# Optimization experiments

Measured on AMD Instinct MI355X. Metric: run time of the kernel, lower is better.

## Reference

```python
import jax, jax.numpy as jnp
import numpy as np


def channel_linear(h, W, b):
    # h: (b, s, n_in, d_channels); W: (d, n_out, n_in); b: (d, n_out)
    out = jnp.einsum('bsic,coi->bsoc', h, W)
    return out + b.T[None, None]  # (b, s, n_out, d)


def setup_inputs() -> dict:
    d, s, bsz = 64, 64, 512
    lt, p = d * (d - 1) // 2, d * d
    key = jax.random.key(0)
    ks = jax.random.split(key, 12)
    inp = {
        'x': jax.random.normal(ks[0], (bsz, d), dtype=jnp.float32),
        'z': jax.random.normal(ks[1], (s, lt + p), dtype=jnp.float32),
    }
    widths = [d, 32, 32, 32, 1]
    for li, (ni, no) in enumerate(zip(widths[:-1], widths[1:])):
        inp[f'W{li}'] = jax.random.normal(ks[2 + 2 * li], (d, no, ni), dtype=jnp.float32) / np.sqrt(ni).astype(np.float32)
        inp[f'b{li}'] = jax.random.normal(ks[3 + 2 * li], (d, no), dtype=jnp.float32) * 0.01
    return inp


def reference(x, z, W0, b0, W1, b1, W2, b2, W3, b3):
    d = x.shape[1]
    s = z.shape[0]
    lt_width = d * (d - 1) // 2
    rows, cols = np.tril_indices(d, -1)  # matches torch.tril_indices(d, d, offset=-1)

    # get_z_adjacency_lt_p: strictly-lower-triangular matrix conjugated by z_p
    z_lt = jnp.zeros((s, d, d), dtype=z.dtype).at[:, rows, cols].set(z[:, :lt_width])
    z_p = z[:, -d * d:].reshape(s, d, d)
    # z_p^T @ z_lt @ z_p
    z_adj = jnp.einsum('sri,srt,stj->sij', z_p, z_lt, z_p)  # (s, d, d)

    # broadcast multiply: h[b,s,i,j] = A[s,i,j] * x[b,i]
    h = z_adj[None, :, :, :] * x[:, None, :, None]  # (b, s, d, d)

    h = jax.nn.relu(channel_linear(h, W0, b0))  # (b, s, 32, d)
    h = jax.nn.relu(channel_linear(h, W1, b1))
    h = jax.nn.relu(channel_linear(h, W2, b2))
    out = jnp.squeeze(channel_linear(h, W3, b3), axis=-2)  # (b, s, d)
    return (out, z_adj)
```

## Files before the change

### kernel.cpp

```cpp
#include <hip/hip_runtime.h>
#include <math.h>

#define D 64
#define S 64
#define BSZ 512
#define LTW 2016
#define ZROW 6112
#define OUT0_SIZE (BSZ * S * D)
#define ZADJ_OFF  OUT0_SIZE

typedef float    f32x4 __attribute__((ext_vector_type(4)));
typedef _Float16 f16x8 __attribute__((ext_vector_type(8)));
typedef _Float16 f16x2 __attribute__((ext_vector_type(2)));

union V8 { f16x8 v; f16x2 h2[4]; uint4 u; };

__device__ __forceinline__ f16x2 pkrtz(float a, float b) {
    return __builtin_bit_cast(f16x2, __builtin_amdgcn_cvt_pkrtz(a, b));
}

__global__ __launch_bounds__(256) void k_zadjprep(
    const float* __restrict__ z, float* __restrict__ zadj,
    const float* __restrict__ x,
    const float* __restrict__ W0, const float* __restrict__ W1,
    const float* __restrict__ W2,
    uint4* __restrict__ w0f, uint4* __restrict__ w1f,
    uint4* __restrict__ w2f, uint4* __restrict__ xf) {
    __shared__ float zp[4096];
    __shared__ float zlt[4160];
    __shared__ float T[1280];
    const int blk = blockIdx.x;
    const int tid = threadIdx.x;

    if (blk < 256) {
        const int s = blk >> 2, jt = blk & 3;
        const float* zs = z + (size_t)s * ZROW;
#pragma unroll
        for (int rep = 0; rep < 16; ++rep) {
            int idx = tid + rep * 256;
            zp[idx] = zs[LTW + idx];
        }
        for (int idx = tid; idx < 4160; idx += 256) zlt[idx] = 0.0f;
        __syncthreads();
        for (int k = tid; k < LTW; k += 256) {
            float kf = (float)k;
            int r = (int)((1.0f + sqrtf(1.0f + 8.0f * kf)) * 0.5f);
            while (r * (r - 1) / 2 > k) --r;
            while ((r + 1) * r / 2 <= k) ++r;
            int t = k - r * (r - 1) / 2;
            zlt[r * 65 + t] = zs[k];
        }
        __syncthreads();
        const int rr = tid & 63, wj = (tid >> 6) * 4;
        {
            f32x4 acc = {0.0f, 0.0f, 0.0f, 0.0f};
            for (int t = 0; t < 64; ++t) {
                float zl = zlt[rr * 65 + t];
                f32x4 zpv = *(const f32x4*)&zp[t * 64 + jt * 16 + wj];
#pragma unroll
                for (int q = 0; q < 4; ++q) acc[q] = fmaf(zl, zpv[q], acc[q]);
            }
            *(f32x4*)&T[rr * 20 + wj] = acc;
        }
        __syncthreads();
        {
            const int i = rr;
            f32x4 acc = {0.0f, 0.0f, 0.0f, 0.0f};
            for (int r = 0; r < 64; ++r) {
                float zv = zp[r * 64 + i];
                f32x4 tv = *(const f32x4*)&T[r * 20 + wj];
#pragma unroll
                for (int q = 0; q < 4; ++q) acc[q] = fmaf(zv, tv[q], acc[q]);
            }
            *(f32x4*)&zadj[(size_t)s * 4096 + i * 64 + jt * 16 + wj] = acc;
        }
    } else {
        const int c = blk - 256;
        const int sl = tid >> 6, ln = tid & 63;
        const int q = ln >> 4, l15 = ln & 15;
        {
            int Mt = sl >> 1, ks = sl & 1;
            const float* src = W0 + c * 2048 + (Mt * 16 + l15) * 64 + ks * 32 + q * 8;
            V8 hv;
#pragma unroll
            for (int j = 0; j < 8; ++j) hv.v[j] = (_Float16)src[j];
            w0f[(size_t)(c * 4 + sl) * 64 + ln] = hv.u;
        }
        {
            const float* Wsrc = (sl < 2) ? W1 : W2;
            uint4* dstb = (sl < 2) ? w1f : w2f;
            int Mt = sl & 1;
            const float* srow = Wsrc + c * 1024 + (Mt * 16 + l15) * 32;
            V8 hi, lo;
#pragma unroll
            for (int j = 0; j < 8; ++j) {
                int k = ((j >> 2) << 4) + q * 4 + (j & 3);
                float e = srow[k];
                _Float16 h = (_Float16)e;
                hi.v[j] = h;
                lo.v[j] = (_Float16)(e - (float)h);
            }
            size_t base = ((size_t)(c * 2 + Mt) * 64 + ln) * 2;
            dstb[base] = hi.u;
            dstb[base + 1] = lo.u;
        }
        if (tid < 64) {
            int f = c * 64 + tid;
            int fln = f & 63, ks = (f >> 6) & 1, bt = f >> 7;
            int n = bt * 16 + (fln & 15), i0 = ks * 32 + (fln >> 4) * 8;
            const float* src = x + n * 64 + i0;
            V8 hv;
#pragma unroll
            for (int j = 0; j < 8; ++j) hv.v[j] = (_Float16)src[j];
            xf[f] = hv.u;
        }
    }
}

__global__ __launch_bounds__(256, 3) void k_main_mfma(
    const uint4* __restrict__ xf, const uint4* __restrict__ w0f,
    const uint4* __restrict__ w1f, const uint4* __restrict__ w2f,
    const float* __restrict__ zadj,
    const float* __restrict__ B0, const float* __restrict__ B1,
    const float* __restrict__ B2, const float* __restrict__ W3,
    const float* __restrict__ B3, float* __restrict__ outT) {
    const int bh = blockIdx.x;
    const int c = blockIdx.y, sg = blockIdx.z;
    const int tid = threadIdx.x;
    const int wave = tid >> 6, lane = tid & 63;
    const int quad = lane >> 4;
    const int btbase = bh * 16 + wave * 4;

    V8 a0[2][2];
#pragma unroll
    for (int Mt = 0; Mt < 2; ++Mt)
#pragma unroll
        for (int ks = 0; ks < 2; ++ks)
            a0[Mt][ks].u = w0f[(size_t)(c * 4 + Mt * 2 + ks) * 64 + lane];
    V8 a1h[2], a1l[2], a2h[2], a2l[2];
#pragma unroll
    for (int Mt = 0; Mt < 2; ++Mt) {
        size_t base = ((size_t)(c * 2 + Mt) * 64 + lane) * 2;
        a1h[Mt].u = w1f[base];
        a1l[Mt].u = w1f[base + 1];
        a2h[Mt].u = w2f[base];
        a2l[Mt].u = w2f[base + 1];
    }
    f32x4 b0v[2], b1v[2], b2v[2], w3v[2];
#pragma unroll
    for (int Mt = 0; Mt < 2; ++Mt) {
        int off = c * 32 + Mt * 16 + quad * 4;
        b0v[Mt] = *(const f32x4*)(B0 + off);
        b1v[Mt] = *(const f32x4*)(B1 + off);
        b2v[Mt] = *(const f32x4*)(B2 + off);
        w3v[Mt] = *(const f32x4*)(W3 + off);
    }
    const float b3v = B3[c];

#pragma unroll 1
    for (int it = 0; it < 4; ++it) {
        const int s = sg * 4 + it;
        f16x2 zvh[2][4];
#pragma unroll
        for (int ks = 0; ks < 2; ++ks) {
            const float* zp = zadj + (size_t)s * 4096 + (ks * 32 + quad * 8) * 64 + c;
            float zv[8];
#pragma unroll
            for (int j = 0; j < 8; ++j) zv[j] = zp[j * 64];
#pragma unroll
            for (int t = 0; t < 4; ++t)
                zvh[ks][t] = pkrtz(zv[2 * t], zv[2 * t + 1]);
        }
        V8 a0s[2][2];
#pragma unroll
        for (int Mt = 0; Mt < 2; ++Mt)
#pragma unroll
            for (int ks = 0; ks < 2; ++ks)
#pragma unroll
                for (int t = 0; t < 4; ++t)
                    a0s[Mt][ks].h2[t] = a0[Mt][ks].h2[t] * zvh[ks][t];

        float red[4];
#pragma unroll
        for (int Nt = 0; Nt < 4; ++Nt) {
            f32x4 acc0[2] = {b0v[0], b0v[1]};
#pragma unroll
            for (int ks = 0; ks < 2; ++ks) {
                V8 xv;
                xv.u = xf[(size_t)((btbase + Nt) * 2 + ks) * 64 + lane];
#pragma unroll
                for (int Mt = 0; Mt < 2; ++Mt)
                    acc0[Mt] = __builtin_amdgcn_mfma_f32_16x16x32_f16(
                        a0s[Mt][ks].v, xv.v, acc0[Mt], 0, 0, 0);
            }
            V8 bb;
            bb.h2[0] = pkrtz(fmaxf(acc0[0][0], 0.0f), fmaxf(acc0[0][1], 0.0f));
            bb.h2[1] = pkrtz(fmaxf(acc0[0][2], 0.0f), fmaxf(acc0[0][3], 0.0f));
            bb.h2[2] = pkrtz(fmaxf(acc0[1][0], 0.0f), fmaxf(acc0[1][1], 0.0f));
            bb.h2[3] = pkrtz(fmaxf(acc0[1][2], 0.0f), fmaxf(acc0[1][3], 0.0f));
            f32x4 acc1[2] = {b1v[0], b1v[1]};
#pragma unroll
            for (int Mt = 0; Mt < 2; ++Mt) {
                acc1[Mt] = __builtin_amdgcn_mfma_f32_16x16x32_f16(
                    a1h[Mt].v, bb.v, acc1[Mt], 0, 0, 0);
                acc1[Mt] = __builtin_amdgcn_mfma_f32_16x16x32_f16(
                    a1l[Mt].v, bb.v, acc1[Mt], 0, 0, 0);
            }
            V8 cc;
            cc.h2[0] = pkrtz(fmaxf(acc1[0][0], 0.0f), fmaxf(acc1[0][1], 0.0f));
            cc.h2[1] = pkrtz(fmaxf(acc1[0][2], 0.0f), fmaxf(acc1[0][3], 0.0f));
            cc.h2[2] = pkrtz(fmaxf(acc1[1][0], 0.0f), fmaxf(acc1[1][1], 0.0f));
            cc.h2[3] = pkrtz(fmaxf(acc1[1][2], 0.0f), fmaxf(acc1[1][3], 0.0f));
            f32x4 acc2[2] = {b2v[0], b2v[1]};
#pragma unroll
            for (int Mt = 0; Mt < 2; ++Mt) {
                acc2[Mt] = __builtin_amdgcn_mfma_f32_16x16x32_f16(
                    a2h[Mt].v, cc.v, acc2[Mt], 0, 0, 0);
                acc2[Mt] = __builtin_amdgcn_mfma_f32_16x16x32_f16(
                    a2l[Mt].v, cc.v, acc2[Mt], 0, 0, 0);
            }
            float p = 0.0f;
#pragma unroll
            for (int Mt = 0; Mt < 2; ++Mt)
#pragma unroll
                for (int r = 0; r < 4; ++r)
                    p = fmaf(w3v[Mt][r], fmaxf(acc2[Mt][r], 0.0f), p);
            p += __shfl_xor(p, 16, 64);
            p += __shfl_xor(p, 32, 64);
            red[Nt] = p;
        }
        float outv = (quad & 2) ? ((quad & 1) ? red[3] : red[2])
                                : ((quad & 1) ? red[1] : red[0]);
        outv += b3v;
        outT[((size_t)s * 64 + c) * 512 + bh * 256 + tid] = outv;
    }
}

__global__ __launch_bounds__(256, 3) void k_main_valu(
    const float* __restrict__ xsrc, const float* __restrict__ zadj,
    const float* __restrict__ W0, const float* __restrict__ B0,
    const float* __restrict__ W1, const float* __restrict__ B1,
    const float* __restrict__ W2, const float* __restrict__ B2,
    const float* __restrict__ W3, const float* __restrict__ B3,
    float* __restrict__ outp, int o_sS, int o_cS, int o_bS) {
    const int c = blockIdx.x;
    const int s = blockIdx.y;
    const int lane = threadIdx.x & 63;
    const int wave = threadIdx.x >> 6;

    const float* w0c = W0 + c * 2048;
    const float* w1c = W1 + c * 1024;
    const float* w2c = W2 + c * 1024;
    const float* w3c = W3 + c * 32;
    const float* b0c = B0 + c * 32;
    const float* b1c = B1 + c * 32;
    const float* b2c = B2 + c * 32;
    const float b3v = B3[c];
    const float* zc = zadj + s * 4096 + c;

#pragma unroll 1
    for (int bc = 0; bc < 2; ++bc) {
        const int b = wave * 128 + bc * 64 + lane;
        float h1[32], h2[32];
#pragma unroll
        for (int o = 0; o < 32; ++o) h1[o] = b0c[o];
#pragma unroll 8
        for (int i = 0; i < 64; ++i) {
            float hi = zc[i * 64] * xsrc[b * 64 + i];
#pragma unroll
            for (int o = 0; o < 32; ++o) h1[o] = fmaf(w0c[o * 64 + i], hi, h1[o]);
        }
#pragma unroll
        for (int o = 0; o < 32; ++o) { h1[o] = fmaxf(h1[o], 0.0f); h2[o] = b1c[o]; }
#pragma unroll 8
        for (int j = 0; j < 32; ++j) {
            float v = h1[j];
#pragma unroll
            for (int o = 0; o < 32; ++o) h2[o] = fmaf(w1c[o * 32 + j], v, h2[o]);
        }
#pragma unroll
        for (int o = 0; o < 32; ++o) { h2[o] = fmaxf(h2[o], 0.0f); h1[o] = b2c[o]; }
#pragma unroll 8
        for (int j = 0; j < 32; ++j) {
            float v = h2[j];
#pragma unroll
            for (int o = 0; o < 32; ++o) h1[o] = fmaf(w2c[o * 32 + j], v, h1[o]);
        }
        float a = b3v;
#pragma unroll
        for (int j = 0; j < 32; ++j) a = fmaf(w3c[j], fmaxf(h1[j], 0.0f), a);
        outp[s * o_sS + c * o_cS + b * o_bS] = a;
    }
}

__global__ __launch_bounds__(256) void k_outT(const float* __restrict__ outT,
                                              float* __restrict__ out) {
    __shared__ float tile[64][65];
    const int bt = blockIdx.x;
    const int s = blockIdx.y;
    const int tid = threadIdx.x;
    const int r0 = tid >> 6, q = tid & 63;
#pragma unroll
    for (int rep = 0; rep < 16; ++rep) {
        int crow = rep * 4 + r0;
        tile[crow][q] = outT[(s * 64 + crow) * 512 + bt * 64 + q];
    }
    __syncthreads();
#pragma unroll
    for (int rep = 0; rep < 16; ++rep) {
        int brow = rep * 4 + r0;
        out[(bt * 64 + brow) * 4096 + s * 64 + q] = tile[q][brow];
    }
}

extern "C" void kernel_launch(void* const* d_in, const int* in_sizes, int n_in,
                              void* d_out, int out_size, void* d_ws, size_t ws_size,
                              hipStream_t stream) {
    const float* x  = (const float*)d_in[0];
    const float* z  = (const float*)d_in[1];
    const float* W0 = (const float*)d_in[2];
    const float* B0 = (const float*)d_in[3];
    const float* W1 = (const float*)d_in[4];
    const float* B1 = (const float*)d_in[5];
    const float* W2 = (const float*)d_in[6];
    const float* B2 = (const float*)d_in[7];
    const float* W3 = (const float*)d_in[8];
    const float* B3 = (const float*)d_in[9];

    float* out  = (float*)d_out;
    float* zadj = out + ZADJ_OFF;

    const size_t OT_B  = (size_t)S * D * BSZ * sizeof(float);
    const size_t XF_B  = 4096 * 16;
    const size_t W0F_B = (size_t)64 * 4 * 64 * 16;
    const size_t W1F_B = (size_t)64 * 2 * 64 * 2 * 16;
    const size_t W2F_B = W1F_B;
    const bool has_oT   = ws_size >= OT_B;
    const bool has_frag = ws_size >= OT_B + XF_B + W0F_B + W1F_B + W2F_B;

    char* wsb = (char*)d_ws;
    float* outT = (float*)wsb;
    uint4* xf   = (uint4*)(wsb + OT_B);
    uint4* w0f  = (uint4*)(wsb + OT_B + XF_B);
    uint4* w1f  = (uint4*)(wsb + OT_B + XF_B + W0F_B);
    uint4* w2f  = (uint4*)(wsb + OT_B + XF_B + W0F_B + W1F_B);

    if (has_frag) {
        hipLaunchKernelGGL(k_zadjprep, dim3(320), dim3(256), 0, stream,
                           z, zadj, x, W0, W1, W2, w0f, w1f, w2f, xf);
        hipLaunchKernelGGL(k_main_mfma, dim3(2, 64, 16), dim3(256), 0, stream,
                           xf, w0f, w1f, w2f, zadj,
                           B0, B1, B2, W3, B3, outT);
        hipLaunchKernelGGL(k_outT, dim3(8, S), dim3(256), 0, stream, outT, out);
    } else {
        hipLaunchKernelGGL(k_zadjprep, dim3(256), dim3(256), 0, stream,
                           z, zadj, x, W0, W1, W2,
                           (uint4*)nullptr, (uint4*)nullptr, (uint4*)nullptr,
                           (uint4*)nullptr);
        float* op = has_oT ? outT : out;
        const int o_sS = has_oT ? (64 * 512) : 64;
        const int o_cS = has_oT ? 512 : 1;
        const int o_bS = has_oT ? 1 : 4096;
        hipLaunchKernelGGL(k_main_valu, dim3(D, S), dim3(256), 0, stream,
                           x, zadj, W0, B0, W1, B1, W2, B2, W3, B3,
                           op, o_sS, o_cS, o_bS);
        if (has_oT)
            hipLaunchKernelGGL(k_outT, dim3(8, S), dim3(256), 0, stream, outT, out);
    }
}
```

Before: 119.4 us.

## Drop fp16 hi/lo split for layers 1-2 and read transposed zadj copy

```diff
diff --git a/kernel.cpp b/kernel.cpp
--- a/kernel.cpp
+++ b/kernel.cpp
@@ -21,6 +21,7 @@
 
 __global__ __launch_bounds__(256) void k_zadjprep(
     const float* __restrict__ z, float* __restrict__ zadj,
+    float* __restrict__ zt,
     const float* __restrict__ x,
     const float* __restrict__ W0, const float* __restrict__ W1,
     const float* __restrict__ W2,
@@ -73,6 +74,11 @@
                 for (int q = 0; q < 4; ++q) acc[q] = fmaf(zv, tv[q], acc[q]);
             }
             *(f32x4*)&zadj[(size_t)s * 4096 + i * 64 + jt * 16 + wj] = acc;
+            if (zt) {
+#pragma unroll
+                for (int q = 0; q < 4; ++q)
+                    zt[(size_t)s * 4096 + (jt * 16 + wj + q) * 64 + i] = acc[q];
+            }
         }
     } else {
         const int c = blk - 256;
@@ -91,18 +97,13 @@
             uint4* dstb = (sl < 2) ? w1f : w2f;
             int Mt = sl & 1;
             const float* srow = Wsrc + c * 1024 + (Mt * 16 + l15) * 32;
-            V8 hi, lo;
+            V8 hv;
 #pragma unroll
             for (int j = 0; j < 8; ++j) {
                 int k = ((j >> 2) << 4) + q * 4 + (j & 3);
-                float e = srow[k];
-                _Float16 h = (_Float16)e;
-                hi.v[j] = h;
-                lo.v[j] = (_Float16)(e - (float)h);
-            }
-            size_t base = ((size_t)(c * 2 + Mt) * 64 + ln) * 2;
-            dstb[base] = hi.u;
-            dstb[base + 1] = lo.u;
+                hv.v[j] = (_Float16)srow[k];
+            }
+            dstb[(size_t)(c * 2 + Mt) * 64 + ln] = hv.u;
         }
         if (tid < 64) {
             int f = c * 64 + tid;
@@ -117,10 +118,11 @@
     }
 }
 
-__global__ __launch_bounds__(256, 3) void k_main_mfma(
+template <bool ZT>
+__global__ __launch_bounds__(256, 4) void k_main_mfma(
     const uint4* __restrict__ xf, const uint4* __restrict__ w0f,
     const uint4* __restrict__ w1f, const uint4* __restrict__ w2f,
-    const float* __restrict__ zadj,
+    const float* __restrict__ zadj, const float* __restrict__ zadjT,
     const float* __restrict__ B0, const float* __restrict__ B1,
     const float* __restrict__ B2, const float* __restrict__ W3,
     const float* __restrict__ B3, float* __restrict__ outT) {
@@ -137,14 +139,11 @@
 #pragma unroll
         for (int ks = 0; ks < 2; ++ks)
             a0[Mt][ks].u = w0f[(size_t)(c * 4 + Mt * 2 + ks) * 64 + lane];
-    V8 a1h[2], a1l[2], a2h[2], a2l[2];
+    V8 a1[2], a2[2];
 #pragma unroll
     for (int Mt = 0; Mt < 2; ++Mt) {
-        size_t base = ((size_t)(c * 2 + Mt) * 64 + lane) * 2;
-        a1h[Mt].u = w1f[base];
-        a1l[Mt].u = w1f[base + 1];
-        a2h[Mt].u = w2f[base];
-        a2l[Mt].u = w2f[base + 1];
+        a1[Mt].u = w1f[(size_t)(c * 2 + Mt) * 64 + lane];
+        a2[Mt].u = w2f[(size_t)(c * 2 + Mt) * 64 + lane];
     }
     f32x4 b0v[2], b1v[2], b2v[2], w3v[2];
 #pragma unroll
@@ -161,15 +160,31 @@
     for (int it = 0; it < 4; ++it) {
         const int s = sg * 4 + it;
         f16x2 zvh[2][4];
-#pragma unroll
-        for (int ks = 0; ks < 2; ++ks) {
-            const float* zp = zadj + (size_t)s * 4096 + (ks * 32 + quad * 8) * 64 + c;
-            float zv[8];
-#pragma unroll
-            for (int j = 0; j < 8; ++j) zv[j] = zp[j * 64];
-#pragma unroll
-            for (int t = 0; t < 4; ++t)
-                zvh[ks][t] = pkrtz(zv[2 * t], zv[2 * t + 1]);
+        if (ZT) {
+            const f32x4* ztp = (const f32x4*)(zadjT + (size_t)s * 4096 + c * 64);
+            f32x4 zq[4];
+            zq[0] = ztp[quad * 2];
+            zq[1] = ztp[quad * 2 + 1];
+            zq[2] = ztp[8 + quad * 2];
+            zq[3] = ztp[8 + quad * 2 + 1];
+#pragma unroll
+            for (int ks = 0; ks < 2; ++ks)
+#pragma unroll
+                for (int t = 0; t < 4; ++t) {
+                    const f32x4& v = zq[ks * 2 + (t >> 1)];
+                    zvh[ks][t] = pkrtz(v[(t & 1) * 2], v[(t & 1) * 2 + 1]);
+                }
+        } else {
+#pragma unroll
+            for (int ks = 0; ks < 2; ++ks) {
+                const float* zp = zadj + (size_t)s * 4096 + (ks * 32 + quad * 8) * 64 + c;
+                float zv[8];
+#pragma unroll
+                for (int j = 0; j < 8; ++j) zv[j] = zp[j * 64];
+#pragma unroll
+                for (int t = 0; t < 4; ++t)
+                    zvh[ks][t] = pkrtz(zv[2 * t], zv[2 * t + 1]);
+            }
         }
         V8 a0s[2][2];
 #pragma unroll
@@ -200,12 +215,9 @@
             bb.h2[3] = pkrtz(fmaxf(acc0[1][2], 0.0f), fmaxf(acc0[1][3], 0.0f));
             f32x4 acc1[2] = {b1v[0], b1v[1]};
 #pragma unroll
-            for (int Mt = 0; Mt < 2; ++Mt) {
+            for (int Mt = 0; Mt < 2; ++Mt)
                 acc1[Mt] = __builtin_amdgcn_mfma_f32_16x16x32_f16(
-                    a1h[Mt].v, bb.v, acc1[Mt], 0, 0, 0);
-                acc1[Mt] = __builtin_amdgcn_mfma_f32_16x16x32_f16(
-                    a1l[Mt].v, bb.v, acc1[Mt], 0, 0, 0);
-            }
+                    a1[Mt].v, bb.v, acc1[Mt], 0, 0, 0);
             V8 cc;
             cc.h2[0] = pkrtz(fmaxf(acc1[0][0], 0.0f), fmaxf(acc1[0][1], 0.0f));
             cc.h2[1] = pkrtz(fmaxf(acc1[0][2], 0.0f), fmaxf(acc1[0][3], 0.0f));
@@ -213,12 +225,9 @@
             cc.h2[3] = pkrtz(fmaxf(acc1[1][2], 0.0f), fmaxf(acc1[1][3], 0.0f));
             f32x4 acc2[2] = {b2v[0], b2v[1]};
 #pragma unroll
-            for (int Mt = 0; Mt < 2; ++Mt) {
+            for (int Mt = 0; Mt < 2; ++Mt)
                 acc2[Mt] = __builtin_amdgcn_mfma_f32_16x16x32_f16(
-                    a2h[Mt].v, cc.v, acc2[Mt], 0, 0, 0);
-                acc2[Mt] = __builtin_amdgcn_mfma_f32_16x16x32_f16(
-                    a2l[Mt].v, cc.v, acc2[Mt], 0, 0, 0);
-            }
+                    a2[Mt].v, cc.v, acc2[Mt], 0, 0, 0);
             float p = 0.0f;
 #pragma unroll
             for (int Mt = 0; Mt < 2; ++Mt)
@@ -333,28 +342,38 @@
     const size_t OT_B  = (size_t)S * D * BSZ * sizeof(float);
     const size_t XF_B  = 4096 * 16;
     const size_t W0F_B = (size_t)64 * 4 * 64 * 16;
-    const size_t W1F_B = (size_t)64 * 2 * 64 * 2 * 16;
+    const size_t W1F_B = (size_t)64 * 2 * 64 * 16;
     const size_t W2F_B = W1F_B;
+    const size_t ZT_B  = (size_t)S * 4096 * sizeof(float);
+    const size_t FRAG_END = OT_B + XF_B + W0F_B + W1F_B + W2F_B;
     const bool has_oT   = ws_size >= OT_B;
-    const bool has_frag = ws_size >= OT_B + XF_B + W0F_B + W1F_B + W2F_B;
+    const bool has_frag = ws_size >= FRAG_END;
+    const bool has_zt   = ws_size >= FRAG_END + ZT_B;
 
     char* wsb = (char*)d_ws;
-    float* outT = (float*)wsb;
-    uint4* xf   = (uint4*)(wsb + OT_B);
-    uint4* w0f  = (uint4*)(wsb + OT_B + XF_B);
-    uint4* w1f  = (uint4*)(wsb + OT_B + XF_B + W0F_B);
-    uint4* w2f  = (uint4*)(wsb + OT_B + XF_B + W0F_B + W1F_B);
+    float* outT  = (float*)wsb;
+    uint4* xf    = (uint4*)(wsb + OT_B);
+    uint4* w0f   = (uint4*)(wsb + OT_B + XF_B);
+    uint4* w1f   = (uint4*)(wsb + OT_B + XF_B + W0F_B);
+    uint4* w2f   = (uint4*)(wsb + OT_B + XF_B + W0F_B + W1F_B);
+    float* zadjT = (float*)(wsb + FRAG_END);
 
     if (has_frag) {
         hipLaunchKernelGGL(k_zadjprep, dim3(320), dim3(256), 0, stream,
-                           z, zadj, x, W0, W1, W2, w0f, w1f, w2f, xf);
-        hipLaunchKernelGGL(k_main_mfma, dim3(2, 64, 16), dim3(256), 0, stream,
-                           xf, w0f, w1f, w2f, zadj,
-                           B0, B1, B2, W3, B3, outT);
+                           z, zadj, has_zt ? zadjT : (float*)nullptr,
+                           x, W0, W1, W2, w0f, w1f, w2f, xf);
+        if (has_zt)
+            hipLaunchKernelGGL((k_main_mfma<true>), dim3(2, 64, 16), dim3(256),
+                               0, stream, xf, w0f, w1f, w2f, zadj, zadjT,
+                               B0, B1, B2, W3, B3, outT);
+        else
+            hipLaunchKernelGGL((k_main_mfma<false>), dim3(2, 64, 16), dim3(256),
+                               0, stream, xf, w0f, w1f, w2f, zadj, zadjT,
+                               B0, B1, B2, W3, B3, outT);
         hipLaunchKernelGGL(k_outT, dim3(8, S), dim3(256), 0, stream, outT, out);
     } else {
         hipLaunchKernelGGL(k_zadjprep, dim3(256), dim3(256), 0, stream,
-                           z, zadj, x, W0, W1, W2,
+                           z, zadj, (float*)nullptr, x, W0, W1, W2,
                            (uint4*)nullptr, (uint4*)nullptr, (uint4*)nullptr,
                            (uint4*)nullptr);
         float* op = has_oT ? outT : out;
```

After: 114.3 us. 4.3% less time.
